# Kernel tuning notes

Hardware: AMD Instinct MI355X
Metric: run time of the kernel (lower is better)

Reference implementation:

```python
import jax, jax.numpy as jnp
import numpy as np
from jax import lax

B, T, D, H = 2048, 512, 8, 80  # batch, seq_len, input_dim, hidden_dim


def setup_inputs() -> dict:
    key = jax.random.key(0)
    ks = jax.random.split(key, 10)
    s = 1.0 / np.sqrt(H)  # torch LSTM init: U(-1/sqrt(H), 1/sqrt(H))
    u = lambda k, shape: jax.random.uniform(k, shape, jnp.float32, -s, s)
    return {
        "X": jax.random.normal(ks[0], (B, T, D), jnp.float32),
        "W_ih0": u(ks[1], (4 * H, D)),
        "W_hh0": u(ks[2], (4 * H, H)),
        "b_ih0": u(ks[3], (4 * H,)),
        "b_hh0": u(ks[4], (4 * H,)),
        "W_ih1": u(ks[5], (4 * H, H)),
        "W_hh1": u(ks[6], (4 * H, H)),
        "b_ih1": u(ks[7], (4 * H,)),
        "b_hh1": u(ks[8], (4 * H,)),
        "X_seq_len": jax.random.randint(ks[9], (B,), 1, T + 1),  # valid lengths in [1, T]
    }


def _lstm_layer(x_tm, W_ih, W_hh, b_ih, b_hh):
    """x_tm: [T, B, Din] time-major. Returns hidden states [T, B, H].
    PyTorch gate order: i, f, g, o."""
    # Precompute all input projections in one big GEMM: [T, B, 4H]
    xg = jnp.einsum('tbd,gd->tbg', x_tm, W_ih) + b_ih + b_hh
    Hd = W_hh.shape[1]
    h0 = jnp.zeros((x_tm.shape[1], Hd), x_tm.dtype)

    def step(carry, g_in):
        h, c = carry
        g = g_in + h @ W_hh.T  # [B, 4H]
        i, f, gg, o = jnp.split(g, 4, axis=-1)
        c = jax.nn.sigmoid(f) * c + jax.nn.sigmoid(i) * jnp.tanh(gg)
        h = jax.nn.sigmoid(o) * jnp.tanh(c)
        return (h, c), h

    _, hs = lax.scan(step, (h0, h0), xg)
    return hs


def reference(X, W_ih0, W_hh0, b_ih0, b_hh0, W_ih1, W_hh1, b_ih1, b_hh1, X_seq_len):
    x = jnp.swapaxes(X, 0, 1)  # [T, B, D] time-major for scan
    h1 = _lstm_layer(x, W_ih0, W_hh0, b_ih0, b_hh0)   # [T, B, H]
    h2 = _lstm_layer(h1, W_ih1, W_hh1, b_ih1, b_hh1)  # [T, B, H]
    # Gather last valid timestep per sequence (packed-seq semantics):
    # state at t = len-1 only depends on inputs <= len-1, so padded run is equivalent.
    idx = X_seq_len - 1
    out = h2[idx, jnp.arange(X.shape[0])]  # [B, H]
    return out
```

## Files before the change

kernel.cpp:

```cpp
#include <hip/hip_runtime.h>
#include <math.h>

#define B_   2048
#define T_   512
#define D_   8
#define H_   80
#define NB   16
#define NBLK (B_ / NB)
#define NTH  640
#define KS0  3
#define KS1  5
#define A0S  256
#define A1S  384
#define A0BUF (16 * A0S)
#define A1BUF (16 * A1S)

typedef float f32x4  __attribute__((ext_vector_type(4)));
typedef short bf16x8 __attribute__((ext_vector_type(8)));
typedef unsigned short u16x4 __attribute__((ext_vector_type(4)));

__device__ __forceinline__ float sigm(float x) {
  return __builtin_amdgcn_rcpf(1.0f + __expf(-x));
}
__device__ __forceinline__ unsigned short f2bf(float f) {
  unsigned u = __builtin_bit_cast(unsigned, f);
  return (unsigned short)((u + 0x7FFFu + ((u >> 16) & 1u)) >> 16);
}
__device__ __forceinline__ float bf2f(unsigned short b) {
  unsigned u = ((unsigned)b) << 16;
  return __builtin_bit_cast(float, u);
}
__device__ __forceinline__ int swz(int row, int byte_in_row) {
  return byte_in_row ^ ((row & 7) << 4);
}
__device__ __forceinline__ float cell(float gi, float gf, float gg, float go,
                                      float& c) {
  float si = sigm(gi), sf = sigm(gf);
  float tg = __builtin_fmaf(2.0f, sigm(2.0f * gg), -1.0f);
  c = sf * c + si * tg;
  float th = __builtin_fmaf(2.0f, sigm(2.0f * c), -1.0f);
  return sigm(go) * th;
}

__global__ __launch_bounds__(512)
void sort_by_len(const int* __restrict__ slen, int* __restrict__ perm) {
  __shared__ int cnt[513];
  const int tid = threadIdx.x;
  for (int i = tid; i < 513; i += 512) cnt[i] = 0;
  __syncthreads();
  for (int b = tid; b < B_; b += 512) atomicAdd(&cnt[T_ - slen[b]], 1);
  __syncthreads();
  if (tid == 0) { int s = 0;
    for (int k = 0; k < 513; ++k) { int c = cnt[k]; cnt[k] = s; s += c; } }
  __syncthreads();
  for (int b = tid; b < B_; b += 512) {
    int pos = atomicAdd(&cnt[T_ - slen[b]], 1);
    perm[pos] = b;
  }
}

__global__ __launch_bounds__(NTH)
void lstm2_mfma(const float* __restrict__ X,
                const float* __restrict__ Wih0, const float* __restrict__ Whh0,
                const float* __restrict__ bih0, const float* __restrict__ bhh0,
                const float* __restrict__ Wih1, const float* __restrict__ Whh1,
                const float* __restrict__ bih1, const float* __restrict__ bhh1,
                const int* __restrict__ slen, const int* __restrict__ perm,
                float* __restrict__ out)
{
  __shared__ char a0lds[2 * A0BUF];
  __shared__ char a1lds[2 * A1BUF];
  __shared__ int  pbs[NB];
  __shared__ int  lns[NB];

  const int tid = threadIdx.x;
  const int w   = tid >> 6;
  const int l   = tid & 63;
  const int lr  = l & 15;
  const int q   = l >> 4;
  const int L   = (w < 5) ? 0 : 1;
  const int v   = w - 5 * L;
  const int u   = 16 * v + lr;

  if (tid < NB) {
    int pb = perm[blockIdx.x * NB + tid];
    pbs[tid] = pb;
    lns[tid] = slen[pb];
  }

  bf16x8 wf[4][KS1];
  float  bias[4];
  if (L == 0) {
    #pragma unroll
    for (int g = 0; g < 4; ++g) {
      const int n = 80 * g + u;
      bias[g] = bih0[n] + bhh0[n];
      #pragma unroll
      for (int ks = 0; ks < KS0; ++ks) {
        bf16x8 vv;
        #pragma unroll
        for (int j = 0; j < 8; ++j) {
          int k = 32 * ks + 8 * q + j;
          float f = (k < 8)  ? Wih0[n * D_ + k]
                  : (k < 16) ? Wih0[n * D_ + (k - 8)]
                             : Whh0[n * H_ + (k - 16)];
          vv[j] = (short)f2bf(f);
        }
        wf[g][ks] = vv;
      }
    }
  } else {
    #pragma unroll
    for (int g = 0; g < 4; ++g) {
      const int n = 80 * g + u;
      bias[g] = bih1[n] + bhh1[n];
      #pragma unroll
      for (int ks = 0; ks < KS1; ++ks) {
        bf16x8 vv;
        #pragma unroll
        for (int j = 0; j < 8; ++j) {
          int k = 32 * ks + 8 * q + j;
          float f = (k < 80) ? Wih1[n * H_ + k] : Whh1[n * H_ + (k - 80)];
          vv[j] = (short)f2bf(f);
        }
        wf[g][ks] = vv;
      }
    }
  }

  for (int i = tid; i < (2 * A0BUF) / 4; i += NTH) ((int*)a0lds)[i] = 0;
  for (int i = tid; i < (2 * A1BUF) / 4; i += NTH) ((int*)a1lds)[i] = 0;
  __syncthreads();

  const int mlen = lns[0];
  int seq4[4], len4[4];
  #pragma unroll
  for (int r = 0; r < 4; ++r) { seq4[r] = pbs[4 * q + r]; len4[r] = lns[4 * q + r]; }

  const int xs = tid >> 4, xt = (tid & 15) >> 1, xh = tid & 1;
  const float* xbase = nullptr;
  f32x4 xa = {}, xb = {};
  if (tid < 256) {
    xbase = X + (size_t)pbs[xs] * (T_ * D_) + 4 * xh;
    int t0 = xt;     if (t0 > T_ - 1) t0 = T_ - 1;
    int t1 = 8 + xt; if (t1 > T_ - 1) t1 = T_ - 1;
    xa = *(const f32x4*)(xbase + t0 * D_);
    xb = *(const f32x4*)(xbase + t1 * D_);
  }
  #pragma unroll
  for (int tt = 0; tt < 2; ++tt) {
    if (tid < 256 && xt == tt) {
      u16x4 hi, lo;
      #pragma unroll
      for (int j = 0; j < 4; ++j) { hi[j] = f2bf(xa[j]); lo[j] = f2bf(xa[j] - bf2f(hi[j])); }
      char* buf = a0lds + tt * A0BUF;
      *(u16x4*)(buf + xs * A0S + swz(xs, 8 * xh))      = hi;
      *(u16x4*)(buf + xs * A0S + swz(xs, 16 + 8 * xh)) = lo;
    }
  }
  __syncthreads();

  float c[4] = {0.f, 0.f, 0.f, 0.f};

  if (L == 0) {
    f32x4 acc[4] = {};
    #pragma unroll
    for (int ks = 0; ks < KS0; ++ks) {
      bf16x8 a = *(const bf16x8*)(a0lds + lr * A0S + swz(lr, 64 * ks + 16 * q));
      #pragma unroll
      for (int g = 0; g < 4; ++g)
        acc[g] = __builtin_amdgcn_mfma_f32_16x16x32_bf16(a, wf[g][ks], acc[g], 0, 0, 0);
    }
    char* A1w = a1lds;
    char* A0w = a0lds + A0BUF;
    #pragma unroll
    for (int r = 0; r < 4; ++r) {
      const int row = 4 * q + r;
      float h = cell(acc[0][r] + bias[0], acc[1][r] + bias[1],
                     acc[2][r] + bias[2], acc[3][r] + bias[3], c[r]);
      unsigned short hb = f2bf(h);
      *(unsigned short*)(A1w + row * A1S + swz(row, 2 * u)) = hb;
      *(unsigned short*)(A0w + row * A0S + swz(row, 32 + 2 * u)) = hb;
    }
  }
  __syncthreads();

  #pragma unroll 2
  for (int i = 0; i < mlen; ++i) {
    const int cur = i & 1, nxt = cur ^ 1;

    if (tid < 256 && ((i + 2) & 7) == 0) {
      xa = xb;
      int tc = i + 10 + xt; if (tc > T_ - 1) tc = T_ - 1;
      xb = *(const f32x4*)(xbase + tc * D_);
    }

    f32x4 acc[4] = {};
    if (L == 1) {
      const char* A1p = a1lds + cur * A1BUF;
      #pragma unroll
      for (int ks = 0; ks < KS1; ++ks) {
        bf16x8 a = *(const bf16x8*)(A1p + lr * A1S + swz(lr, 64 * ks + 16 * q));
        #pragma unroll
        for (int g = 0; g < 4; ++g)
          acc[g] = __builtin_amdgcn_mfma_f32_16x16x32_bf16(a, wf[g][ks], acc[g], 0, 0, 0);
      }
    } else {
      const char* A0p = a0lds + nxt * A0BUF;
      #pragma unroll
      for (int ks = 0; ks < KS0; ++ks) {
        bf16x8 a = *(const bf16x8*)(A0p + lr * A0S + swz(lr, 64 * ks + 16 * q));
        #pragma unroll
        for (int g = 0; g < 4; ++g)
          acc[g] = __builtin_amdgcn_mfma_f32_16x16x32_bf16(a, wf[g][ks], acc[g], 0, 0, 0);
      }
    }

    if (tid < 256 && xt == ((i + 2) & 7)) {
      u16x4 hi, lo;
      #pragma unroll
      for (int j = 0; j < 4; ++j) { hi[j] = f2bf(xa[j]); lo[j] = f2bf(xa[j] - bf2f(hi[j])); }
      char* buf = a0lds + cur * A0BUF;
      *(u16x4*)(buf + xs * A0S + swz(xs, 8 * xh))      = hi;
      *(u16x4*)(buf + xs * A0S + swz(xs, 16 + 8 * xh)) = lo;
    }

    char* A1n = a1lds + nxt * A1BUF;
    char* A0c = a0lds + cur * A0BUF;

    if (L == 1) {
      #pragma unroll
      for (int r = 0; r < 4; ++r) {
        const int row = 4 * q + r;
        float h = cell(acc[0][r] + bias[0], acc[1][r] + bias[1],
                       acc[2][r] + bias[2], acc[3][r] + bias[3], c[r]);
        *(unsigned short*)(A1n + row * A1S + swz(row, 160 + 2 * u)) = f2bf(h);
        if (i == len4[r] - 1) out[(size_t)seq4[r] * H_ + u] = h;
      }
    } else {
      #pragma unroll
      for (int r = 0; r < 4; ++r) {
        const int row = 4 * q + r;
        float h = cell(acc[0][r] + bias[0], acc[1][r] + bias[1],
                       acc[2][r] + bias[2], acc[3][r] + bias[3], c[r]);
        unsigned short hb = f2bf(h);
        *(unsigned short*)(A1n + row * A1S + swz(row, 2 * u)) = hb;
        *(unsigned short*)(A0c + row * A0S + swz(row, 32 + 2 * u)) = hb;
      }
    }
    __syncthreads();
  }
}

extern "C" void kernel_launch(void* const* d_in, const int* in_sizes, int n_in,
                              void* d_out, int out_size, void* d_ws, size_t ws_size,
                              hipStream_t stream) {
  const float* X    = (const float*)d_in[0];
  const float* Wih0 = (const float*)d_in[1];
  const float* Whh0 = (const float*)d_in[2];
  const float* bih0 = (const float*)d_in[3];
  const float* bhh0 = (const float*)d_in[4];
  const float* Wih1 = (const float*)d_in[5];
  const float* Whh1 = (const float*)d_in[6];
  const float* bih1 = (const float*)d_in[7];
  const float* bhh1 = (const float*)d_in[8];
  const int*   slen = (const int*)d_in[9];
  int* perm = (int*)d_ws;

  sort_by_len<<<1, 512, 0, stream>>>(slen, perm);
  lstm2_mfma<<<NBLK, NTH, 0, stream>>>(
      X, Wih0, Whh0, bih0, bhh0, Wih1, Whh1, bih1, bhh1, slen, perm,
      (float*)d_out);
}
```

Baseline: 735.0 us.

## Fold exp2 scaling into weights and transpose MFMA for vectorized h stores

Pre-scales the gate weights and biases by log2(e), or 2*log2(e) for the g gate, so the cell can use raw exp2. The cell math is rewritten to share reciprocals: the four gate nonlinearities and the cell update need fewer rcp calls, and tanh(c) uses an abs/copysign form. The MFMA operands are swapped, so each lane now holds four consecutive hidden units for one sequence row. This lets h be written to LDS as a single 8-byte vector and the output as one float4 instead of scattered scalar stores. The risk is that fusing products into one reciprocal can overflow for large gate inputs, and scaling the weights before bf16 rounding slightly changes precision.

```diff
diff --git a/kernel.cpp b/kernel.cpp
--- a/kernel.cpp
+++ b/kernel.cpp
@@ -14,13 +14,19 @@
 #define A1S  384
 #define A0BUF (16 * A0S)
 #define A1BUF (16 * A1S)
+#define LOG2E 1.44269504f
+#define K2    2.88539008f
 
 typedef float f32x4  __attribute__((ext_vector_type(4)));
 typedef short bf16x8 __attribute__((ext_vector_type(8)));
 typedef unsigned short u16x4 __attribute__((ext_vector_type(4)));
 
-__device__ __forceinline__ float sigm(float x) {
-  return __builtin_amdgcn_rcpf(1.0f + __expf(-x));
+__device__ __forceinline__ float E2(float x) {
+#if __has_builtin(__builtin_amdgcn_exp2f)
+  return __builtin_amdgcn_exp2f(x);
+#else
+  return __expf(x * 0.6931471806f);
+#endif
 }
 __device__ __forceinline__ unsigned short f2bf(float f) {
   unsigned u = __builtin_bit_cast(unsigned, f);
@@ -33,13 +39,18 @@
 __device__ __forceinline__ int swz(int row, int byte_in_row) {
   return byte_in_row ^ ((row & 7) << 4);
 }
-__device__ __forceinline__ float cell(float gi, float gf, float gg, float go,
+__device__ __forceinline__ float cell(float ai, float af, float ag, float ao,
                                       float& c) {
-  float si = sigm(gi), sf = sigm(gf);
-  float tg = __builtin_fmaf(2.0f, sigm(2.0f * gg), -1.0f);
-  c = sf * c + si * tg;
-  float th = __builtin_fmaf(2.0f, sigm(2.0f * c), -1.0f);
-  return sigm(go) * th;
+  const float ei = E2(-ai), ef = E2(-af), eg = E2(-ag), eo = E2(-ao);
+  const float P  = (1.0f + ei) * (1.0f + eg);
+  const float pf = 1.0f + ef;
+  const float cn = __builtin_fmaf(c, P, (1.0f - eg) * pf)
+                 * __builtin_amdgcn_rcpf(P * pf);
+  c = cn;
+  const float ec = E2(-K2 * fabsf(cn));
+  const float t  = (1.0f - ec)
+                 * __builtin_amdgcn_rcpf((1.0f + eo) * (1.0f + ec));
+  return copysignf(t, cn);
 }
 
 __global__ __launch_bounds__(512)
@@ -81,6 +92,7 @@
   const int L   = (w < 5) ? 0 : 1;
   const int v   = w - 5 * L;
   const int u   = 16 * v + lr;
+  const int ub4 = 16 * v + 4 * q;
 
   if (tid < NB) {
     int pb = perm[blockIdx.x * NB + tid];
@@ -89,12 +101,17 @@
   }
 
   bf16x8 wf[4][KS1];
-  float  bias[4];
+  float  bias[4][4];
   if (L == 0) {
     #pragma unroll
     for (int g = 0; g < 4; ++g) {
+      const float sc = (g == 2) ? K2 : LOG2E;
       const int n = 80 * g + u;
-      bias[g] = bih0[n] + bhh0[n];
+      #pragma unroll
+      for (int r = 0; r < 4; ++r) {
+        const int nb = 80 * g + ub4 + r;
+        bias[g][r] = (bih0[nb] + bhh0[nb]) * sc;
+      }
       #pragma unroll
       for (int ks = 0; ks < KS0; ++ks) {
         bf16x8 vv;
@@ -104,7 +121,7 @@
           float f = (k < 8)  ? Wih0[n * D_ + k]
                   : (k < 16) ? Wih0[n * D_ + (k - 8)]
                              : Whh0[n * H_ + (k - 16)];
-          vv[j] = (short)f2bf(f);
+          vv[j] = (short)f2bf(f * sc);
         }
         wf[g][ks] = vv;
       }
@@ -112,8 +129,13 @@
   } else {
     #pragma unroll
     for (int g = 0; g < 4; ++g) {
+      const float sc = (g == 2) ? K2 : LOG2E;
       const int n = 80 * g + u;
-      bias[g] = bih1[n] + bhh1[n];
+      #pragma unroll
+      for (int r = 0; r < 4; ++r) {
+        const int nb = 80 * g + ub4 + r;
+        bias[g][r] = (bih1[nb] + bhh1[nb]) * sc;
+      }
       #pragma unroll
       for (int ks = 0; ks < KS1; ++ks) {
         bf16x8 vv;
@@ -121,7 +143,7 @@
         for (int j = 0; j < 8; ++j) {
           int k = 32 * ks + 8 * q + j;
           float f = (k < 80) ? Wih1[n * H_ + k] : Whh1[n * H_ + (k - 80)];
-          vv[j] = (short)f2bf(f);
+          vv[j] = (short)f2bf(f * sc);
         }
         wf[g][ks] = vv;
       }
@@ -132,10 +154,9 @@
   for (int i = tid; i < (2 * A1BUF) / 4; i += NTH) ((int*)a1lds)[i] = 0;
   __syncthreads();
 
-  const int mlen = lns[0];
-  int seq4[4], len4[4];
-  #pragma unroll
-  for (int r = 0; r < 4; ++r) { seq4[r] = pbs[4 * q + r]; len4[r] = lns[4 * q + r]; }
+  const int mlen  = lns[0];
+  const int pbseq = pbs[lr];
+  const int lm1   = lns[lr] - 1;
 
   const int xs = tid >> 4, xt = (tid & 15) >> 1, xh = tid & 1;
   const float* xbase = nullptr;
@@ -169,19 +190,19 @@
       bf16x8 a = *(const bf16x8*)(a0lds + lr * A0S + swz(lr, 64 * ks + 16 * q));
       #pragma unroll
       for (int g = 0; g < 4; ++g)
-        acc[g] = __builtin_amdgcn_mfma_f32_16x16x32_bf16(a, wf[g][ks], acc[g], 0, 0, 0);
+        acc[g] = __builtin_amdgcn_mfma_f32_16x16x32_bf16(wf[g][ks], a, acc[g], 0, 0, 0);
     }
     char* A1w = a1lds;
     char* A0w = a0lds + A0BUF;
+    u16x4 hv;
     #pragma unroll
     for (int r = 0; r < 4; ++r) {
-      const int row = 4 * q + r;
-      float h = cell(acc[0][r] + bias[0], acc[1][r] + bias[1],
-                     acc[2][r] + bias[2], acc[3][r] + bias[3], c[r]);
-      unsigned short hb = f2bf(h);
-      *(unsigned short*)(A1w + row * A1S + swz(row, 2 * u)) = hb;
-      *(unsigned short*)(A0w + row * A0S + swz(row, 32 + 2 * u)) = hb;
-    }
+      float h = cell(acc[0][r] + bias[0][r], acc[1][r] + bias[1][r],
+                     acc[2][r] + bias[2][r], acc[3][r] + bias[3][r], c[r]);
+      hv[r] = f2bf(h);
+    }
+    *(u16x4*)(A1w + lr * A1S + swz(lr, 2 * ub4))      = hv;
+    *(u16x4*)(A0w + lr * A0S + swz(lr, 32 + 2 * ub4)) = hv;
   }
   __syncthreads();
 
@@ -203,7 +224,7 @@
         bf16x8 a = *(const bf16x8*)(A1p + lr * A1S + swz(lr, 64 * ks + 16 * q));
         #pragma unroll
         for (int g = 0; g < 4; ++g)
-          acc[g] = __builtin_amdgcn_mfma_f32_16x16x32_bf16(a, wf[g][ks], acc[g], 0, 0, 0);
+          acc[g] = __builtin_amdgcn_mfma_f32_16x16x32_bf16(wf[g][ks], a, acc[g], 0, 0, 0);
       }
     } else {
       const char* A0p = a0lds + nxt * A0BUF;
@@ -212,7 +233,7 @@
         bf16x8 a = *(const bf16x8*)(A0p + lr * A0S + swz(lr, 64 * ks + 16 * q));
         #pragma unroll
         for (int g = 0; g < 4; ++g)
-          acc[g] = __builtin_amdgcn_mfma_f32_16x16x32_bf16(a, wf[g][ks], acc[g], 0, 0, 0);
+          acc[g] = __builtin_amdgcn_mfma_f32_16x16x32_bf16(wf[g][ks], a, acc[g], 0, 0, 0);
       }
     }
 
@@ -229,24 +250,27 @@
     char* A0c = a0lds + cur * A0BUF;
 
     if (L == 1) {
-      #pragma unroll
-      for (int r = 0; r < 4; ++r) {
-        const int row = 4 * q + r;
-        float h = cell(acc[0][r] + bias[0], acc[1][r] + bias[1],
-                       acc[2][r] + bias[2], acc[3][r] + bias[3], c[r]);
-        *(unsigned short*)(A1n + row * A1S + swz(row, 160 + 2 * u)) = f2bf(h);
-        if (i == len4[r] - 1) out[(size_t)seq4[r] * H_ + u] = h;
-      }
+      float h[4];
+      u16x4 hv;
+      #pragma unroll
+      for (int r = 0; r < 4; ++r) {
+        h[r] = cell(acc[0][r] + bias[0][r], acc[1][r] + bias[1][r],
+                    acc[2][r] + bias[2][r], acc[3][r] + bias[3][r], c[r]);
+        hv[r] = f2bf(h[r]);
+      }
+      *(u16x4*)(A1n + lr * A1S + swz(lr, 160 + 2 * ub4)) = hv;
+      if (i == lm1)
+        *(f32x4*)(out + (size_t)pbseq * H_ + ub4) = (f32x4){h[0], h[1], h[2], h[3]};
     } else {
-      #pragma unroll
-      for (int r = 0; r < 4; ++r) {
-        const int row = 4 * q + r;
-        float h = cell(acc[0][r] + bias[0], acc[1][r] + bias[1],
-                       acc[2][r] + bias[2], acc[3][r] + bias[3], c[r]);
-        unsigned short hb = f2bf(h);
-        *(unsigned short*)(A1n + row * A1S + swz(row, 2 * u)) = hb;
-        *(unsigned short*)(A0c + row * A0S + swz(row, 32 + 2 * u)) = hb;
-      }
+      u16x4 hv;
+      #pragma unroll
+      for (int r = 0; r < 4; ++r) {
+        float h = cell(acc[0][r] + bias[0][r], acc[1][r] + bias[1][r],
+                       acc[2][r] + bias[2][r], acc[3][r] + bias[3][r], c[r]);
+        hv[r] = f2bf(h);
+      }
+      *(u16x4*)(A1n + lr * A1S + swz(lr, 2 * ub4))      = hv;
+      *(u16x4*)(A0c + lr * A0S + swz(lr, 32 + 2 * ub4)) = hv;
     }
     __syncthreads();
   }
```

After: 598.7 us, median of 2. -18.6%, faster.
